# Optimization experiments

Hardware: AMD Instinct MI355X
Metric: run time of the kernel (lower is better)

## Reference

```python
import jax, jax.numpy as jnp
import numpy as np

DIM = 1152
N_HEADS = 12
GROUPS = 6
KV_HEADS = N_HEADS // GROUPS  # 2
HEAD_DIM = DIM // N_HEADS     # 96
BASE = 10000.0
BSZ = 4
SEQ = 2048
MAX_SEQ = 2048
NEG_INF = -1e9


def rope(x, start_pos):
    # x: [b, s, h, d]; interleaved (even/odd) rotary embedding, matching the torch code
    b, s, h, d = x.shape
    x_even = x[..., 0::2]
    x_odd = x[..., 1::2]
    # even positions <- -x_odd, odd positions <- x_even (interleaved)
    x_rev = jnp.stack([-x_odd, x_even], axis=-1).reshape(x.shape)
    i = jnp.repeat(jnp.arange(0, d, 2), 2).astype(x.dtype)  # [d]
    theta = 1.0 / (BASE ** (i / d))                          # [d]
    pos = jnp.arange(start_pos + s, dtype=x.dtype)           # [s] (start_pos=0 case, as in source)
    ang = pos[:, None] * theta[None, :]                      # [s, d]
    cos = jnp.cos(ang).reshape(1, s, 1, d)
    sin = jnp.sin(ang).reshape(1, s, 1, d)
    return x * cos + x_rev * sin


def setup_inputs() -> dict:
    key = jax.random.key(0)
    ks = jax.random.split(key, 4)
    sc = 0.02
    x = jax.random.normal(ks[0], (BSZ, SEQ, DIM), jnp.float32)
    # causal mask [S, end_pos]: 0 on/below diagonal, large negative above
    mask = jnp.triu(jnp.full((SEQ, SEQ), NEG_INF, jnp.float32), k=1)
    q_w = jax.random.normal(ks[1], (DIM, DIM), jnp.float32) * sc
    q_b = jnp.zeros((DIM,), jnp.float32)
    kv_w = jax.random.normal(ks[2], (2 * KV_HEADS * HEAD_DIM, DIM), jnp.float32) * sc
    kv_b = jnp.zeros((2 * KV_HEADS * HEAD_DIM,), jnp.float32)
    wo_w = jax.random.normal(ks[3], (DIM, DIM), jnp.float32) * sc
    wo_b = jnp.zeros((DIM,), jnp.float32)
    return {"x": x, "mask": mask, "q_w": q_w, "q_b": q_b, "kv_w": kv_w,
            "kv_b": kv_b, "wo_w": wo_w, "wo_b": wo_b, "start_pos": 0}


def reference(x, mask, q_w, q_b, kv_w, kv_b, wo_w, wo_b, start_pos):
    b, s, f = x.shape
    end = start_pos + s
    q = (x @ q_w.T + q_b).reshape(b, s, N_HEADS, HEAD_DIM)
    kv = (x @ kv_w.T + kv_b).reshape(b, s, 2, KV_HEADS, HEAD_DIM)
    k, v = kv[:, :, 0], kv[:, :, 1]
    rq = rope(q, start_pos)
    rk = rope(k, start_pos)
    # KV-cache write (cache initialized to zeros, as in the buffer)
    k_cache = jnp.zeros((b, MAX_SEQ, KV_HEADS, HEAD_DIM), x.dtype).at[:, start_pos:end].set(rk)
    v_cache = jnp.zeros((b, MAX_SEQ, KV_HEADS, HEAD_DIM), x.dtype).at[:, start_pos:end].set(v)
    # repeat_kv: head index = kv_head * groups + g  -> jnp.repeat along head axis
    kk = jnp.repeat(k_cache[:, :end], GROUPS, axis=2)  # [b, t, H, d]
    vv = jnp.repeat(v_cache[:, :end], GROUPS, axis=2)
    scale = HEAD_DIM ** -0.5
    attn = jnp.einsum('bshd,bthd->bsht', rq, kk) * scale
    attn = attn + mask[:, None, :]  # mask [s, t] -> [s, 1, t] broadcast over b, h
    scores = jax.nn.softmax(attn.astype(jnp.float32), axis=-1).astype(x.dtype)
    out = jnp.einsum('bsht,bthd->bshd', scores, vv).reshape(b, s, DIM)
    return out @ wo_w.T + wo_b
```

## Files before the change

### kernel.cpp

```cpp
#include <hip/hip_runtime.h>
#include <hip/hip_bf16.h>

constexpr int DIMD  = 1152;
constexpr int NHD   = 12;
constexpr int KVHD  = 2;
constexpr int HDD   = 96;
constexpr int GRPS  = 6;
constexpr int SEQL  = 2048;
constexpr int BSZ4  = 4;
constexpr int MROWS = BSZ4 * SEQL;
constexpr int NQKV  = DIMD + 2 * KVHD * HDD;
constexpr float SCALE = 0.10206207261596577f;

typedef short  bf16x8 __attribute__((ext_vector_type(8)));
typedef float  f32x4  __attribute__((ext_vector_type(4)));

typedef __attribute__((address_space(3))) unsigned int       lds_u32_t;
typedef __attribute__((address_space(1))) const unsigned int glb_u32_t;

__device__ __forceinline__ void gload16(const unsigned short* g, unsigned short* l) {
    __builtin_amdgcn_global_load_lds((glb_u32_t*)(const void*)g,
                                     (lds_u32_t*)(void*)l, 16, 0, 0);
}

__device__ __forceinline__ unsigned short f2bf(float f) {
    unsigned int u = __builtin_bit_cast(unsigned int, f);
    u += 0x7fff + ((u >> 16) & 1);
    return (unsigned short)(u >> 16);
}

__device__ __forceinline__ unsigned cvtpk(float a, float b) {
    unsigned r;
    asm volatile("v_cvt_pk_bf16_f32 %0, %1, %2" : "=v"(r) : "v"(a), "v"(b));
    return r;
}

__device__ __forceinline__ void cvt4(const float4* __restrict__ s,
                                     ushort4* __restrict__ d, int i) {
    float4 f = s[i];
    ushort4 o;
    o.x = f2bf(f.x); o.y = f2bf(f.y); o.z = f2bf(f.z); o.w = f2bf(f.w);
    d[i] = o;
}

__global__ __launch_bounds__(256) void prep_kernel(
    const float4* __restrict__ x,   const float4* __restrict__ qw,
    const float4* __restrict__ kvw, const float4* __restrict__ wow,
    ushort4* __restrict__ xb,   ushort4* __restrict__ qwb,
    ushort4* __restrict__ kvwb, ushort4* __restrict__ wowb,
    const int* __restrict__ sp, float2* __restrict__ tab)
{
    constexpr int X4  = MROWS * DIMD / 4;
    constexpr int W4  = DIMD * DIMD / 4;
    constexpr int KV4 = 2 * KVHD * HDD * DIMD / 4;
    constexpr int NT  = SEQL * 48;
    int i = blockIdx.x * 256 + threadIdx.x;
    if (i < X4)  { cvt4(x, xb, i); return; }
    i -= X4;
    if (i < W4)  { cvt4(qw, qwb, i); return; }
    i -= W4;
    if (i < KV4) { cvt4(kvw, kvwb, i); return; }
    i -= KV4;
    if (i < W4)  { cvt4(wow, wowb, i); return; }
    i -= W4;
    if (i < NT) {
        int s = i / 48, j = i - (i / 48) * 48;
        float th = powf(10000.0f, -(float)(2 * j) / 96.0f);
        float ang = (float)(s + *sp) * th;
        float sn, cs; sincosf(ang, &sn, &cs);
        tab[i] = make_float2(cs, sn);
    }
}

__global__ __launch_bounds__(256) void qkv_mfma_kernel(
    const unsigned short* __restrict__ xb,  const unsigned short* __restrict__ qwb,
    const unsigned short* __restrict__ kvwb,
    const float* __restrict__ qb,  const float* __restrict__ kvb,
    const float2* __restrict__ tab,
    unsigned short* __restrict__ Qo, unsigned short* __restrict__ Ko,
    unsigned short* __restrict__ VTo)
{
    __shared__ __align__(16) unsigned short As[3][128 * 32];
    __shared__ __align__(16) unsigned short Bs[3][128 * 32];

    const int tid  = threadIdx.x;
    const int w    = tid >> 6;
    const int lane = tid & 63;
    const int l16  = lane & 15;
    const int quad = lane >> 4;
    const int wm   = w >> 1, wn = w & 1;

    const int flat = (int)(blockIdx.y * gridDim.x + blockIdx.x);
    const int swz  = (flat & 7) * 96 + (flat >> 3);
    const int m0   = (swz / 12) * 128;
    const int n0   = (swz % 12) * 128;

    const unsigned short* Abase = xb + (size_t)m0 * DIMD;
    const unsigned short* Bbase = (n0 < DIMD)
        ? qwb  + (size_t)n0 * DIMD
        : kvwb + (size_t)(n0 - DIMD) * DIMD;

    const int srow = w * 16 + (lane >> 2);
    const int scol = (lane & 3) * 8;

    f32x4 acc[4][4];
    #pragma unroll
    for (int mi = 0; mi < 4; mi++)
        #pragma unroll
        for (int ni = 0; ni < 4; ni++) acc[mi][ni] = (f32x4){0.f, 0.f, 0.f, 0.f};

    constexpr int NK = DIMD / 32;

    gload16(Abase + (size_t)srow        * DIMD + scol, &As[0][w * 512]);
    gload16(Abase + (size_t)(srow + 64) * DIMD + scol, &As[0][2048 + w * 512]);
    gload16(Bbase + (size_t)srow        * DIMD + scol, &Bs[0][w * 512]);
    gload16(Bbase + (size_t)(srow + 64) * DIMD + scol, &Bs[0][2048 + w * 512]);
    gload16(Abase + (size_t)srow        * DIMD + 32 + scol, &As[1][w * 512]);
    gload16(Abase + (size_t)(srow + 64) * DIMD + 32 + scol, &As[1][2048 + w * 512]);
    gload16(Bbase + (size_t)srow        * DIMD + 32 + scol, &Bs[1][w * 512]);
    gload16(Bbase + (size_t)(srow + 64) * DIMD + 32 + scol, &Bs[1][2048 + w * 512]);

    for (int kt = 0; kt < NK; kt++) {
        const int cur = kt % 3;
        if (kt + 2 < NK) {
            const int stg = (kt + 2) % 3;
            const int k0  = (kt + 2) * 32;
            gload16(Abase + (size_t)srow        * DIMD + k0 + scol, &As[stg][w * 512]);
            gload16(Abase + (size_t)(srow + 64) * DIMD + k0 + scol, &As[stg][2048 + w * 512]);
            gload16(Bbase + (size_t)srow        * DIMD + k0 + scol, &Bs[stg][w * 512]);
            gload16(Bbase + (size_t)(srow + 64) * DIMD + k0 + scol, &Bs[stg][2048 + w * 512]);
            asm volatile("s_waitcnt vmcnt(8)" ::: "memory");
        } else if (kt + 1 < NK) {
            asm volatile("s_waitcnt vmcnt(4)" ::: "memory");
        } else {
            asm volatile("s_waitcnt vmcnt(0)" ::: "memory");
        }
        __builtin_amdgcn_s_barrier();
        asm volatile("" ::: "memory");

        bf16x8 af[4], bfr[4];
        #pragma unroll
        for (int mi = 0; mi < 4; mi++)
            af[mi] = *(const bf16x8*)&As[cur][(wm * 64 + mi * 16 + l16) * 32 + quad * 8];
        #pragma unroll
        for (int ni = 0; ni < 4; ni++)
            bfr[ni] = *(const bf16x8*)&Bs[cur][(wn * 64 + ni * 16 + l16) * 32 + quad * 8];
        #pragma unroll
        for (int mi = 0; mi < 4; mi++)
            #pragma unroll
            for (int ni = 0; ni < 4; ni++)
                acc[mi][ni] = __builtin_amdgcn_mfma_f32_16x16x32_bf16(
                    af[mi], bfr[ni], acc[mi][ni], 0, 0, 0);

        asm volatile("" ::: "memory");
        __builtin_amdgcn_s_barrier();
    }

    #pragma unroll
    for (int ni = 0; ni < 4; ni++) {
        const int n   = n0 + wn * 64 + ni * 16 + l16;
        const bool isQ = (n < DIMD);
        const int jj  = n - DIMD;
        const bool isK = !isQ && (jj < KVHD * HDD);
        const int d   = isQ ? (n % HDD) : (jj % HDD);
        const int hh  = isQ ? (n / HDD) : ((jj / HDD) & 1);
        const float bias = isQ ? qb[n] : kvb[jj];
        const bool doRope = isQ || isK;
        const int de2 = (d >> 1);
        const float sg = (n & 1) ? 1.0f : -1.0f;
        #pragma unroll
        for (int mi = 0; mi < 4; mi++) {
            #pragma unroll
            for (int r = 0; r < 4; r++) {
                const int m = m0 + wm * 64 + mi * 16 + quad * 4 + r;
                const int b = m >> 11;
                const int s = m & (SEQL - 1);
                float v  = acc[mi][ni][r] + bias;
                float pv = __shfl_xor(v, 1, 64);
                float o = v;
                if (doRope) {
                    float2 cs2 = tab[s * 48 + de2];
                    o = v * cs2.x + sg * pv * cs2.y;
                }
                if (isQ)
                    Qo[(((size_t)b * NHD + hh) * SEQL + s) * HDD + d] = f2bf(o);
                else if (isK)
                    Ko[(((size_t)b * KVHD + hh) * SEQL + s) * HDD + d] = f2bf(o);
                else
                    VTo[(((size_t)b * KVHD + hh) * HDD + d) * SEQL + s] = f2bf(o);
            }
        }
    }
}

__global__ __launch_bounds__(256, 3) void attn_mfma_kernel(
    const unsigned short* __restrict__ Q, const unsigned short* __restrict__ K,
    const unsigned short* __restrict__ VT, unsigned short* __restrict__ AO)
{
    constexpr int KHALF = 64 * 104;
    __shared__ __align__(16) unsigned short Ks[2 * KHALF];
    __shared__ __align__(16) unsigned short VTs[96 * 72];
    __shared__ __align__(16) unsigned short Ps[4][16 * 72];
    __shared__ float Al[4][16];

    const int tid  = threadIdx.x;
    const int w    = tid >> 6;
    const int lane = tid & 63;
    const int l16  = lane & 15;
    const int quad = lane >> 4;

    const int idx = (int)blockIdx.x;
    const int qi  = idx / 48;
    const int hb  = idx - qi * 48;
    const int qt  = 31 - qi;
    const int h   = hb % NHD;
    const int b   = hb / NHD;
    const int kvh = h / GRPS;
    const int nkb = qt + 1;

    const unsigned short* Qbase  = Q  + (((size_t)b * NHD  + h)   * SEQL) * HDD;
    const unsigned short* Kbase  = K  + (((size_t)b * KVHD + kvh) * SEQL) * HDD;
    const unsigned short* VTbase = VT + (((size_t)b * KVHD + kvh) * HDD)  * SEQL;

    int goff[7]; int gkind[7]; int loff[7];
    #pragma unroll
    for (int j = 0; j < 7; j++) {
        const int i = w + 4 * j;
        gkind[j] = 2; goff[j] = 0; loff[j] = 0;
        if (i < 13) {
            int slot = i * 64 + lane;
            int r = slot / 13, g = slot - r * 13;
            goff[j]  = r * HDD + (g < 12 ? g * 8 : 0);
            gkind[j] = 0;
            loff[j]  = i * 512;
        } else if (i < 27) {
            int iv = i - 13;
            int slot = iv * 64 + lane;
            if (slot < 864) {
                int r = slot / 9, g = slot - r * 9;
                goff[j]  = r * SEQL + (g < 8 ? g * 8 : 0);
                gkind[j] = 1;
                loff[j]  = iv * 512;
            }
        }
    }

    bf16x8 qf[3];
    {
        const int qrow = qt * 64 + w * 16 + l16;
        const unsigned short* qp = Qbase + (size_t)qrow * HDD + quad * 8;
        qf[0] = *(const bf16x8*)(qp);
        qf[1] = *(const bf16x8*)(qp + 32);
        qf[2] = *(const bf16x8*)(qp + 64);
    }

    float m_r = -1e30f, l_r = 0.0f;
    f32x4 oacc[6];
    #pragma unroll
    for (int nn = 0; nn < 6; nn++) oacc[nn] = (f32x4){0.f, 0.f, 0.f, 0.f};

    #pragma unroll
    for (int j = 0; j < 7; j++)
        if (gkind[j] == 0)
            gload16(Kbase + goff[j], &Ks[loff[j]]);
    #pragma unroll
    for (int j = 0; j < 7; j++)
        if (gkind[j] == 1) {
            if ((w + 4 * j) < 26 || lane < 32)
                gload16(VTbase + goff[j], &VTs[loff[j]]);
        }

    const int dql = w * 16 + l16;

    for (int kb = 0; kb < nkb; kb++) {
        const int  cur  = kb & 1;
        const bool more = (kb + 1 < nkb);

        if (more) {
            const size_t kg = (size_t)(kb + 1) * 64 * HDD;
            #pragma unroll
            for (int j = 0; j < 7; j++)
                if (gkind[j] == 0)
                    gload16(Kbase + kg + goff[j], &Ks[(cur ^ 1) * KHALF + loff[j]]);
            asm volatile("s_waitcnt vmcnt(6)" ::: "memory");
        } else {
            asm volatile("s_waitcnt vmcnt(3)" ::: "memory");
        }
        __builtin_amdgcn_s_barrier();
        asm volatile("" ::: "memory");

        const unsigned short* ksb = &Ks[cur * KHALF];
        f32x4 s[4];
        __builtin_amdgcn_s_setprio(1);
        #pragma unroll
        for (int n = 0; n < 4; n++) {
            const unsigned short* kr = ksb + (n * 16 + l16) * 104 + quad * 8;
            bf16x8 kf0 = *(const bf16x8*)(kr);
            bf16x8 kf1 = *(const bf16x8*)(kr + 32);
            bf16x8 kf2 = *(const bf16x8*)(kr + 64);
            f32x4 a = (f32x4){0.f, 0.f, 0.f, 0.f};
            a = __builtin_amdgcn_mfma_f32_16x16x32_bf16(kf0, qf[0], a, 0, 0, 0);
            a = __builtin_amdgcn_mfma_f32_16x16x32_bf16(kf1, qf[1], a, 0, 0, 0);
            a = __builtin_amdgcn_mfma_f32_16x16x32_bf16(kf2, qf[2], a, 0, 0, 0);
            s[n] = a;
        }
        __builtin_amdgcn_s_setprio(0);

        float v[4][4];
        float mx = -3e30f;
        if (!more) {
            #pragma unroll
            for (int n = 0; n < 4; n++)
                #pragma unroll
                for (int r = 0; r < 4; r++) {
                    float x = s[n][r] * SCALE;
                    if (n * 16 + quad * 4 + r > dql) x = -1e30f;
                    v[n][r] = x;
                    mx = fmaxf(mx, x);
                }
        } else {
            #pragma unroll
            for (int n = 0; n < 4; n++)
                #pragma unroll
                for (int r = 0; r < 4; r++) {
                    float x = s[n][r] * SCALE;
                    v[n][r] = x;
                    mx = fmaxf(mx, x);
                }
        }
        mx = fmaxf(mx, __shfl_xor(mx, 16, 64));
        mx = fmaxf(mx, __shfl_xor(mx, 32, 64));
        const float mnew = fmaxf(m_r, mx);
        const float al = __expf(m_r - mnew);
        if (quad == 0) Al[w][l16] = al;
        float sum = 0.0f;
        #pragma unroll
        for (int n = 0; n < 4; n++) {
            float p0 = __expf(v[n][0] - mnew);
            float p1 = __expf(v[n][1] - mnew);
            float p2 = __expf(v[n][2] - mnew);
            float p3 = __expf(v[n][3] - mnew);
            sum += (p0 + p1) + (p2 + p3);
            uint2 pk;
            pk.x = cvtpk(p0, p1);
            pk.y = cvtpk(p2, p3);
            *(uint2*)&Ps[w][l16 * 72 + n * 16 + quad * 4] = pk;
        }
        sum += __shfl_xor(sum, 16, 64);
        sum += __shfl_xor(sum, 32, 64);
        l_r = l_r * al + sum;
        m_r = mnew;
        __builtin_amdgcn_wave_barrier();

        const float4 alb = *(const float4*)&Al[w][quad * 4];
        bf16x8 pa0 = *(const bf16x8*)&Ps[w][l16 * 72 + quad * 8];
        bf16x8 pa1 = *(const bf16x8*)&Ps[w][l16 * 72 + 32 + quad * 8];
        const float albr[4] = {alb.x, alb.y, alb.z, alb.w};

        if (more) asm volatile("s_waitcnt vmcnt(3)" ::: "memory");
        else      asm volatile("s_waitcnt vmcnt(0)" ::: "memory");
        __builtin_amdgcn_s_barrier();
        asm volatile("" ::: "memory");

        __builtin_amdgcn_s_setprio(1);
        #pragma unroll
        for (int nn = 0; nn < 6; nn++) {
            const unsigned short* vr = &VTs[(nn * 16 + l16) * 72 + quad * 8];
            bf16x8 vb0 = *(const bf16x8*)(vr);
            bf16x8 vb1 = *(const bf16x8*)(vr + 32);
            f32x4 a = oacc[nn];
            #pragma unroll
            for (int r = 0; r < 4; r++) a[r] *= albr[r];
            a = __builtin_amdgcn_mfma_f32_16x16x32_bf16(pa0, vb0, a, 0, 0, 0);
            a = __builtin_amdgcn_mfma_f32_16x16x32_bf16(pa1, vb1, a, 0, 0, 0);
            oacc[nn] = a;
        }
        __builtin_amdgcn_s_setprio(0);

        asm volatile("" ::: "memory");
        __builtin_amdgcn_s_barrier();
        asm volatile("" ::: "memory");

        if (more) {
            const int kg = (kb + 1) * 64;
            #pragma unroll
            for (int j = 0; j < 7; j++)
                if (gkind[j] == 1) {
                    if ((w + 4 * j) < 26 || lane < 32)
                        gload16(VTbase + kg + goff[j], &VTs[loff[j]]);
                }
        }
    }

    const float linv = 1.0f / l_r;
    if (quad == 0) Al[w][l16] = linv;
    __builtin_amdgcn_wave_barrier();
    const float4 lb4 = *(const float4*)&Al[w][quad * 4];
    const float lbr[4] = {lb4.x, lb4.y, lb4.z, lb4.w};
    const int row0 = qt * 64 + w * 16 + quad * 4;
    #pragma unroll
    for (int nn = 0; nn < 6; nn++) {
        #pragma unroll
        for (int r = 0; r < 4; r++) {
            AO[((size_t)b * SEQL + row0 + r) * DIMD + h * HDD + nn * 16 + l16] =
                f2bf(oacc[nn][r] * lbr[r]);
        }
    }
}

__global__ __launch_bounds__(256) void out_mfma_kernel(
    const unsigned short* __restrict__ Ab, const unsigned short* __restrict__ Wb,
    const float* __restrict__ wob, float* __restrict__ out)
{
    __shared__ __align__(16) unsigned short As[3][128 * 32];
    __shared__ __align__(16) unsigned short Bs[3][128 * 32];

    const int tid  = threadIdx.x;
    const int w    = tid >> 6;
    const int lane = tid & 63;
    const int l16  = lane & 15;
    const int quad = lane >> 4;
    const int wm   = w >> 1, wn = w & 1;

    const int flat = (int)(blockIdx.y * gridDim.x + blockIdx.x);
    const int swz  = (flat & 7) * 72 + (flat >> 3);
    const int m0   = (swz / 9) * 128;
    const int n0   = (swz % 9) * 128;

    const unsigned short* Abase = Ab + (size_t)m0 * DIMD;
    const unsigned short* Bbase = Wb + (size_t)n0 * DIMD;

    const int srow = w * 16 + (lane >> 2);
    const int scol = (lane & 3) * 8;

    f32x4 acc[4][4];
    #pragma unroll
    for (int mi = 0; mi < 4; mi++)
        #pragma unroll
        for (int ni = 0; ni < 4; ni++) acc[mi][ni] = (f32x4){0.f, 0.f, 0.f, 0.f};

    constexpr int NK = DIMD / 32;

    gload16(Abase + (size_t)srow        * DIMD + scol, &As[0][w * 512]);
    gload16(Abase + (size_t)(srow + 64) * DIMD + scol, &As[0][2048 + w * 512]);
    gload16(Bbase + (size_t)srow        * DIMD + scol, &Bs[0][w * 512]);
    gload16(Bbase + (size_t)(srow + 64) * DIMD + scol, &Bs[0][2048 + w * 512]);
    gload16(Abase + (size_t)srow        * DIMD + 32 + scol, &As[1][w * 512]);
    gload16(Abase + (size_t)(srow + 64) * DIMD + 32 + scol, &As[1][2048 + w * 512]);
    gload16(Bbase + (size_t)srow        * DIMD + 32 + scol, &Bs[1][w * 512]);
    gload16(Bbase + (size_t)(srow + 64) * DIMD + 32 + scol, &Bs[1][2048 + w * 512]);

    for (int kt = 0; kt < NK; kt++) {
        const int cur = kt % 3;
        if (kt + 2 < NK) {
            const int stg = (kt + 2) % 3;
            const int k0  = (kt + 2) * 32;
            gload16(Abase + (size_t)srow        * DIMD + k0 + scol, &As[stg][w * 512]);
            gload16(Abase + (size_t)(srow + 64) * DIMD + k0 + scol, &As[stg][2048 + w * 512]);
            gload16(Bbase + (size_t)srow        * DIMD + k0 + scol, &Bs[stg][w * 512]);
            gload16(Bbase + (size_t)(srow + 64) * DIMD + k0 + scol, &Bs[stg][2048 + w * 512]);
            asm volatile("s_waitcnt vmcnt(8)" ::: "memory");
        } else if (kt + 1 < NK) {
            asm volatile("s_waitcnt vmcnt(4)" ::: "memory");
        } else {
            asm volatile("s_waitcnt vmcnt(0)" ::: "memory");
        }
        __builtin_amdgcn_s_barrier();
        asm volatile("" ::: "memory");

        bf16x8 af[4], bfr[4];
        #pragma unroll
        for (int mi = 0; mi < 4; mi++)
            af[mi] = *(const bf16x8*)&As[cur][(wm * 64 + mi * 16 + l16) * 32 + quad * 8];
        #pragma unroll
        for (int ni = 0; ni < 4; ni++)
            bfr[ni] = *(const bf16x8*)&Bs[cur][(wn * 64 + ni * 16 + l16) * 32 + quad * 8];
        #pragma unroll
        for (int mi = 0; mi < 4; mi++)
            #pragma unroll
            for (int ni = 0; ni < 4; ni++)
                acc[mi][ni] = __builtin_amdgcn_mfma_f32_16x16x32_bf16(
                    af[mi], bfr[ni], acc[mi][ni], 0, 0, 0);

        asm volatile("" ::: "memory");
        __builtin_amdgcn_s_barrier();
    }

    #pragma unroll
    for (int ni = 0; ni < 4; ni++) {
        const int n = n0 + wn * 64 + ni * 16 + l16;
        const float bias = wob[n];
        #pragma unroll
        for (int mi = 0; mi < 4; mi++) {
            #pragma unroll
            for (int r = 0; r < 4; r++) {
                const int m = m0 + wm * 64 + mi * 16 + quad * 4 + r;
                out[(size_t)m * DIMD + n] = acc[mi][ni][r] + bias;
            }
        }
    }
}

extern "C" void kernel_launch(void* const* d_in, const int* in_sizes, int n_in,
                              void* d_out, int out_size, void* d_ws, size_t ws_size,
                              hipStream_t stream)
{
    const float* x   = (const float*)d_in[0];
    const float* qw  = (const float*)d_in[2];
    const float* qb  = (const float*)d_in[3];
    const float* kvw = (const float*)d_in[4];
    const float* kvb = (const float*)d_in[5];
    const float* wow = (const float*)d_in[6];
    const float* wob = (const float*)d_in[7];
    const int*   sp  = (const int*)d_in[8];

    const size_t xN   = (size_t)MROWS * DIMD;
    const size_t qwN  = (size_t)DIMD * DIMD;
    const size_t kvwN = (size_t)2 * KVHD * HDD * DIMD;
    const size_t qN   = (size_t)BSZ4 * NHD  * SEQL * HDD;
    const size_t kvN  = (size_t)BSZ4 * KVHD * SEQL * HDD;

    unsigned short* xb   = (unsigned short*)d_ws;
    unsigned short* qwb  = xb   + xN;
    unsigned short* kvwb = qwb  + qwN;
    unsigned short* wowb = kvwb + kvwN;
    unsigned short* Q16  = wowb + qwN;
    unsigned short* K16  = Q16  + qN;
    unsigned short* VT16 = K16  + kvN;
    unsigned short* AO16 = VT16 + kvN;
    float2* tab = (float2*)AO16;

    constexpr int PREP_TOT = (MROWS * DIMD + 2 * DIMD * DIMD
                              + 2 * KVHD * HDD * DIMD) / 4 + SEQL * 48;
    prep_kernel<<<(PREP_TOT + 255) / 256, 256, 0, stream>>>(
        (const float4*)x, (const float4*)qw, (const float4*)kvw, (const float4*)wow,
        (ushort4*)xb, (ushort4*)qwb, (ushort4*)kvwb, (ushort4*)wowb, sp, tab);

    qkv_mfma_kernel<<<dim3(NQKV / 128, MROWS / 128, 1), 256, 0, stream>>>(
        xb, qwb, kvwb, qb, kvb, tab, Q16, K16, VT16);
    attn_mfma_kernel<<<dim3((SEQL / 64) * NHD * BSZ4, 1, 1), 256, 0, stream>>>(
        Q16, K16, VT16, AO16);
    out_mfma_kernel<<<dim3(DIMD / 128, MROWS / 128, 1), 256, 0, stream>>>(
        AO16, wowb, wob, (float*)d_out);
}
```

Measured before the change: 288.8 us.

## Use exp2 with prescaled logits, lazy rescaling, and KV-grouped block order

Folds log2(e) into the score scale so the softmax can call the raw v_exp_f32 instruction instead of __expf. Skips the running-max update and the output-accumulator rescale unless some row's new max exceeds the stored max by more than a threshold (8 in log2 units), which removes per-iteration multiplies on the O accumulators. Remaps block indices so that the six query heads sharing one KV head, and the same batch, are launched next to each other, with the aim of better L2 reuse of K/V tiles. The lazy rescale relies on bounded growth of the unnormalised exponent sums; the final normalisation stays exact.

```diff
diff --git a/kernel.cpp b/kernel.cpp
--- a/kernel.cpp
+++ b/kernel.cpp
@@ -11,6 +11,7 @@
 constexpr int MROWS = BSZ4 * SEQL;
 constexpr int NQKV  = DIMD + 2 * KVHD * HDD;
 constexpr float SCALE = 0.10206207261596577f;
+constexpr float SCALE2 = 0.10206207261596577f * 1.4426950408889634f;
 
 typedef short  bf16x8 __attribute__((ext_vector_type(8)));
 typedef float  f32x4  __attribute__((ext_vector_type(4)));
@@ -32,6 +33,12 @@
 __device__ __forceinline__ unsigned cvtpk(float a, float b) {
     unsigned r;
     asm volatile("v_cvt_pk_bf16_f32 %0, %1, %2" : "=v"(r) : "v"(a), "v"(b));
+    return r;
+}
+
+__device__ __forceinline__ float ex2(float x) {
+    float r;
+    asm volatile("v_exp_f32 %0, %1" : "=v"(r) : "v"(x));
     return r;
 }
 
@@ -209,14 +216,16 @@
     const int l16  = lane & 15;
     const int quad = lane >> 4;
 
-    const int idx = (int)blockIdx.x;
-    const int qi  = idx / 48;
-    const int hb  = idx - qi * 48;
-    const int qt  = 31 - qi;
-    const int h   = hb % NHD;
-    const int b   = hb / NHD;
-    const int kvh = h / GRPS;
-    const int nkb = qt + 1;
+    const int idx  = (int)blockIdx.x;
+    const int grp  = idx & 7;
+    const int j    = idx >> 3;
+    const int jq   = j / 6;
+    const int hrem = j - jq * 6;
+    const int qt   = 31 - jq;
+    const int b    = grp >> 1;
+    const int kvh  = grp & 1;
+    const int h    = kvh * GRPS + hrem;
+    const int nkb  = qt + 1;
 
     const unsigned short* Qbase  = Q  + (((size_t)b * NHD  + h)   * SEQL) * HDD;
     const unsigned short* Kbase  = K  + (((size_t)b * KVHD + kvh) * SEQL) * HDD;
@@ -224,23 +233,23 @@
 
     int goff[7]; int gkind[7]; int loff[7];
     #pragma unroll
-    for (int j = 0; j < 7; j++) {
-        const int i = w + 4 * j;
-        gkind[j] = 2; goff[j] = 0; loff[j] = 0;
+    for (int jj = 0; jj < 7; jj++) {
+        const int i = w + 4 * jj;
+        gkind[jj] = 2; goff[jj] = 0; loff[jj] = 0;
         if (i < 13) {
             int slot = i * 64 + lane;
             int r = slot / 13, g = slot - r * 13;
-            goff[j]  = r * HDD + (g < 12 ? g * 8 : 0);
-            gkind[j] = 0;
-            loff[j]  = i * 512;
+            goff[jj]  = r * HDD + (g < 12 ? g * 8 : 0);
+            gkind[jj] = 0;
+            loff[jj]  = i * 512;
         } else if (i < 27) {
             int iv = i - 13;
             int slot = iv * 64 + lane;
             if (slot < 864) {
                 int r = slot / 9, g = slot - r * 9;
-                goff[j]  = r * SEQL + (g < 8 ? g * 8 : 0);
-                gkind[j] = 1;
-                loff[j]  = iv * 512;
+                goff[jj]  = r * SEQL + (g < 8 ? g * 8 : 0);
+                gkind[jj] = 1;
+                loff[jj]  = iv * 512;
             }
         }
     }
@@ -260,14 +269,14 @@
     for (int nn = 0; nn < 6; nn++) oacc[nn] = (f32x4){0.f, 0.f, 0.f, 0.f};
 
     #pragma unroll
-    for (int j = 0; j < 7; j++)
-        if (gkind[j] == 0)
-            gload16(Kbase + goff[j], &Ks[loff[j]]);
-    #pragma unroll
-    for (int j = 0; j < 7; j++)
-        if (gkind[j] == 1) {
-            if ((w + 4 * j) < 26 || lane < 32)
-                gload16(VTbase + goff[j], &VTs[loff[j]]);
+    for (int jj = 0; jj < 7; jj++)
+        if (gkind[jj] == 0)
+            gload16(Kbase + goff[jj], &Ks[loff[jj]]);
+    #pragma unroll
+    for (int jj = 0; jj < 7; jj++)
+        if (gkind[jj] == 1) {
+            if ((w + 4 * jj) < 26 || lane < 32)
+                gload16(VTbase + goff[jj], &VTs[loff[jj]]);
         }
 
     const int dql = w * 16 + l16;
@@ -279,9 +288,9 @@
         if (more) {
             const size_t kg = (size_t)(kb + 1) * 64 * HDD;
             #pragma unroll
-            for (int j = 0; j < 7; j++)
-                if (gkind[j] == 0)
-                    gload16(Kbase + kg + goff[j], &Ks[(cur ^ 1) * KHALF + loff[j]]);
+            for (int jj = 0; jj < 7; jj++)
+                if (gkind[jj] == 0)
+                    gload16(Kbase + kg + goff[jj], &Ks[(cur ^ 1) * KHALF + loff[jj]]);
             asm volatile("s_waitcnt vmcnt(6)" ::: "memory");
         } else {
             asm volatile("s_waitcnt vmcnt(3)" ::: "memory");
@@ -313,7 +322,7 @@
             for (int n = 0; n < 4; n++)
                 #pragma unroll
                 for (int r = 0; r < 4; r++) {
-                    float x = s[n][r] * SCALE;
+                    float x = s[n][r] * SCALE2;
                     if (n * 16 + quad * 4 + r > dql) x = -1e30f;
                     v[n][r] = x;
                     mx = fmaxf(mx, x);
@@ -323,23 +332,28 @@
             for (int n = 0; n < 4; n++)
                 #pragma unroll
                 for (int r = 0; r < 4; r++) {
-                    float x = s[n][r] * SCALE;
+                    float x = s[n][r] * SCALE2;
                     v[n][r] = x;
                     mx = fmaxf(mx, x);
                 }
         }
         mx = fmaxf(mx, __shfl_xor(mx, 16, 64));
         mx = fmaxf(mx, __shfl_xor(mx, 32, 64));
-        const float mnew = fmaxf(m_r, mx);
-        const float al = __expf(m_r - mnew);
-        if (quad == 0) Al[w][l16] = al;
+
+        const bool resc = !__all(mx <= m_r + 8.0f);
+        float mnew = m_r, al = 1.0f;
+        if (resc) {
+            mnew = fmaxf(m_r, mx);
+            al = ex2(m_r - mnew);
+            if (quad == 0) Al[w][l16] = al;
+        }
         float sum = 0.0f;
         #pragma unroll
         for (int n = 0; n < 4; n++) {
-            float p0 = __expf(v[n][0] - mnew);
-            float p1 = __expf(v[n][1] - mnew);
-            float p2 = __expf(v[n][2] - mnew);
-            float p3 = __expf(v[n][3] - mnew);
+            float p0 = ex2(v[n][0] - mnew);
+            float p1 = ex2(v[n][1] - mnew);
+            float p2 = ex2(v[n][2] - mnew);
+            float p3 = ex2(v[n][3] - mnew);
             sum += (p0 + p1) + (p2 + p3);
             uint2 pk;
             pk.x = cvtpk(p0, p1);
@@ -352,15 +366,22 @@
         m_r = mnew;
         __builtin_amdgcn_wave_barrier();
 
-        const float4 alb = *(const float4*)&Al[w][quad * 4];
         bf16x8 pa0 = *(const bf16x8*)&Ps[w][l16 * 72 + quad * 8];
         bf16x8 pa1 = *(const bf16x8*)&Ps[w][l16 * 72 + 32 + quad * 8];
-        const float albr[4] = {alb.x, alb.y, alb.z, alb.w};
 
         if (more) asm volatile("s_waitcnt vmcnt(3)" ::: "memory");
         else      asm volatile("s_waitcnt vmcnt(0)" ::: "memory");
         __builtin_amdgcn_s_barrier();
         asm volatile("" ::: "memory");
+
+        if (resc) {
+            const float4 alb = *(const float4*)&Al[w][quad * 4];
+            const float albr[4] = {alb.x, alb.y, alb.z, alb.w};
+            #pragma unroll
+            for (int nn = 0; nn < 6; nn++)
+                #pragma unroll
+                for (int r = 0; r < 4; r++) oacc[nn][r] *= albr[r];
+        }
 
         __builtin_amdgcn_s_setprio(1);
         #pragma unroll
@@ -369,8 +390,6 @@
             bf16x8 vb0 = *(const bf16x8*)(vr);
             bf16x8 vb1 = *(const bf16x8*)(vr + 32);
             f32x4 a = oacc[nn];
-            #pragma unroll
-            for (int r = 0; r < 4; r++) a[r] *= albr[r];
             a = __builtin_amdgcn_mfma_f32_16x16x32_bf16(pa0, vb0, a, 0, 0, 0);
             a = __builtin_amdgcn_mfma_f32_16x16x32_bf16(pa1, vb1, a, 0, 0, 0);
             oacc[nn] = a;
@@ -384,10 +403,10 @@
         if (more) {
             const int kg = (kb + 1) * 64;
             #pragma unroll
-            for (int j = 0; j < 7; j++)
-                if (gkind[j] == 1) {
-                    if ((w + 4 * j) < 26 || lane < 32)
-                        gload16(VTbase + kg + goff[j], &VTs[loff[j]]);
+            for (int jj = 0; jj < 7; jj++)
+                if (gkind[jj] == 1) {
+                    if ((w + 4 * jj) < 26 || lane < 32)
+                        gload16(VTbase + kg + goff[jj], &VTs[loff[jj]]);
                 }
         }
     }
```

New measurement: 284.8 us. No clear change (-1.4%).
